# Kernel optimization log

Measured on AMD Instinct MI355X. Metric: run time of the kernel, lower is better.

Reference implementation:

```python
import jax, jax.numpy as jnp
import numpy as np

N = 100000
E = 3200000
EMBED = 64
RBF = 16
EPS_ANGLE = 1e-8
EPS_NORM = 1e-12  # F.normalize default eps


def _linear(h, W, b):
    return h @ W + b


def setup_inputs() -> dict:
    key = jax.random.key(0)
    ks = jax.random.split(key, 12)
    s = lambda fan_in: 1.0 / np.sqrt(fan_in)
    return {
        "x": jax.random.normal(ks[0], (N, EMBED), jnp.float32),
        "coord": jax.random.normal(ks[1], (N, 3), jnp.float32),
        "rbf_feature": jax.random.normal(ks[2], (E, RBF), jnp.float32),
        "edge_index": jax.random.randint(ks[3], (2, E), 0, N, jnp.int64),
        # edge_mlp: Linear(RBF+1, EMBED) -> SiLU -> Linear(EMBED, EMBED)
        "W1": jax.random.uniform(ks[4], (RBF + 1, EMBED), jnp.float32, -s(RBF + 1), s(RBF + 1)),
        "b1": jnp.zeros((EMBED,), jnp.float32),
        "W2": jax.random.uniform(ks[5], (EMBED, EMBED), jnp.float32, -s(EMBED), s(EMBED)),
        "b2": jnp.zeros((EMBED,), jnp.float32),
        # update_mlp: Linear(EMBED, EMBED) -> SiLU -> Linear(EMBED, EMBED)
        "W3": jax.random.uniform(ks[6], (EMBED, EMBED), jnp.float32, -s(EMBED), s(EMBED)),
        "b3": jnp.zeros((EMBED,), jnp.float32),
        "W4": jax.random.uniform(ks[7], (EMBED, EMBED), jnp.float32, -s(EMBED), s(EMBED)),
        "b4": jnp.zeros((EMBED,), jnp.float32),
    }


def reference(x, coord, rbf_feature, edge_index, W1, b1, W2, b2, W3, b3, W4, b4):
    row, col = edge_index[0], edge_index[1]
    # gather per-edge displacement vectors: [E, 3]
    v = coord[row] - coord[col]
    # compute_angle(v, -v): normalize both, cosine, clamp, acos
    norm = jnp.maximum(jnp.linalg.norm(v, axis=-1, keepdims=True), EPS_NORM)
    vn = v / norm
    cos_angle = jnp.clip(jnp.sum(vn * (-vn), axis=-1), -1.0 + EPS_ANGLE, 1.0 - EPS_ANGLE)
    angle = jnp.arccos(cos_angle)[:, None]  # [E, 1]
    edge_feat = jnp.concatenate([rbf_feature, angle], axis=-1)  # [E, RBF+1]
    # edge MLP
    edge_msg = _linear(jax.nn.silu(_linear(edge_feat, W1, b1)), W2, b2)  # [E, EMBED]
    # scatter-add to source nodes (index_add_ over row)
    agg = jax.ops.segment_sum(edge_msg, row, num_segments=x.shape[0])  # [N, EMBED]
    # node update
    return x + _linear(jax.nn.silu(_linear(agg, W3, b3)), W4, b4)
```

## Files before the change

kernel.cpp:

```cpp
#include <hip/hip_runtime.h>
#include <hip/hip_fp16.h>
#include <hip/hip_bf16.h>

typedef __attribute__((ext_vector_type(8)))  short bf16x8;
typedef __attribute__((ext_vector_type(4)))  float f32x4;
typedef __attribute__((ext_vector_type(16))) float f32x16;

constexpr int EMBED = 64;
constexpr int RBF   = 16;

__device__ __forceinline__ short f2bf(float f) {
    __hip_bfloat16 h = __float2bfloat16(f);
    return *reinterpret_cast<short*>(&h);
}
__device__ __forceinline__ float bf2f(short s) {
    unsigned u = ((unsigned)(unsigned short)s) << 16;
    return __uint_as_float(u);
}
__device__ __forceinline__ unsigned pk_bf(float lo, float hi) {
    unsigned l = (unsigned short)f2bf(lo);
    unsigned h = (unsigned short)f2bf(hi);
    return l | (h << 16);
}
__device__ __forceinline__ unsigned pk_f16(float lo, float hi) {
    __half2 h = __halves2half2(__float2half_rn(lo), __float2half_rn(hi));
    return *reinterpret_cast<unsigned*>(&h);
}
__device__ __forceinline__ void atom_pk_add_f16(__half* addr, unsigned data) {
    asm volatile("global_atomic_pk_add_f16 %0, %1, off"
                 :: "v"(addr), "v"(data) : "memory");
}
__device__ __forceinline__ float silu(float x) {
    return x * __builtin_amdgcn_rcpf(1.0f + __expf(-x));
}

constexpr float PI_BF  = 3.140625f;
constexpr float PI2_BF = 1.5703125f;

__device__ __forceinline__ int crow(int j, int h) {
    return (j & 3) + 8 * (j >> 2) + 4 * h;
}

template <bool GUARD, bool F16>
__global__ __launch_bounds__(256, 2) void edge_kernel32(
    const float* __restrict__ rbf,
    const int* __restrict__ ei,
    const float* __restrict__ W1,
    const float* __restrict__ b1,
    const float* __restrict__ W2,
    const float* __restrict__ b2,
    void* __restrict__ agg,
    int e_base, int E)
{
    __shared__ __align__(16) short lds_s[4][32 * 64];
    __shared__ int lds_row[256];
    __shared__ unsigned char lds_flag[256];
    __shared__ int wave_any[4];

    const int tid  = threadIdx.x;
    const int lane = tid & 63;
    const int wave = tid >> 6;
    const int n = lane & 31;
    const int h = lane >> 5;
    const int blk_e0 = e_base + blockIdx.x * 256;

    {
        const int e = blk_e0 + tid;
        const bool v = !GUARD || (e < E);
        const int row = v ? ei[e] : 0;
        const int col = v ? ei[E + e] : 1;
        lds_row[tid]  = row;
        const bool fl = v && (row == col);
        lds_flag[tid] = fl;
        const unsigned long long m = __ballot(fl);
        if (lane == 0) wave_any[wave] = (m != 0ull);
    }
    __syncthreads();

    bf16x8 b1f[2];
    float  b1v[2], dlt[2], b2v[2];
#pragma unroll
    for (int hh = 0; hh < 2; ++hh) {
        const int ch = 2 * n + hh;
#pragma unroll
        for (int j = 0; j < 8; ++j)
            b1f[hh][j] = f2bf(W1[(h * 8 + j) * EMBED + ch]);
        const float w16 = bf2f(f2bf(W1[RBF * EMBED + ch]));
        b1v[hh] = b1[ch] + PI_BF * w16;
        dlt[hh] = (PI2_BF - PI_BF) * w16;
        b2v[hh] = b2[ch];
    }
    bf16x8 b2f[4][2];
#pragma unroll
    for (int kk = 0; kk < 4; ++kk)
#pragma unroll
        for (int hh = 0; hh < 2; ++hh) {
            const int ch = 2 * n + hh;
#pragma unroll
            for (int j = 0; j < 8; ++j)
                b2f[kk][hh][j] = f2bf(W2[(kk * 16 + h * 8 + j) * EMBED + ch]);
        }

    char* const sl = reinterpret_cast<char*>(lds_s[wave]);

#pragma unroll 1
    for (int mt = 0; mt < 2; ++mt) {
        const int e0  = blk_e0 + wave * 64 + mt * 32;
        if (GUARD && e0 >= E) break;
        const int el0 = wave * 64 + mt * 32;

        bf16x8 a1 = {};
        {
            const int ea = e0 + n;
            if (!GUARD || ea < E) {
                const float4 p0 = *reinterpret_cast<const float4*>(rbf + (long long)ea * RBF + h * 8);
                const float4 p1 = *reinterpret_cast<const float4*>(rbf + (long long)ea * RBF + h * 8 + 4);
                a1[0] = f2bf(p0.x); a1[1] = f2bf(p0.y); a1[2] = f2bf(p0.z); a1[3] = f2bf(p0.w);
                a1[4] = f2bf(p1.x); a1[5] = f2bf(p1.y); a1[6] = f2bf(p1.z); a1[7] = f2bf(p1.w);
            }
        }

        f32x16 accA, accB;
#pragma unroll
        for (int j = 0; j < 16; ++j) { accA[j] = b1v[0]; accB[j] = b1v[1]; }
        accA = __builtin_amdgcn_mfma_f32_32x32x16_bf16(a1, b1f[0], accA, 0, 0, 0);
        accB = __builtin_amdgcn_mfma_f32_32x32x16_bf16(a1, b1f[1], accB, 0, 0, 0);

        if (wave_any[wave]) {
#pragma unroll
            for (int j = 0; j < 16; ++j) {
                const int m = crow(j, h);
                if (lds_flag[el0 + m]) { accA[j] += dlt[0]; accB[j] += dlt[1]; }
            }
        }

#pragma unroll
        for (int j = 0; j < 16; ++j) {
            const int m = crow(j, h);
            const unsigned u = pk_bf(silu(accA[j]), silu(accB[j]));
            *reinterpret_cast<unsigned*>(sl + m * 128 + ((4 * n) ^ ((m & 7) << 4))) = u;
        }
        __builtin_amdgcn_wave_barrier();

        f32x16 acc2A, acc2B;
#pragma unroll
        for (int j = 0; j < 16; ++j) { acc2A[j] = b2v[0]; acc2B[j] = b2v[1]; }
#pragma unroll
        for (int kk = 0; kk < 4; ++kk) {
            const int byte = n * 128 + ((kk * 32 + h * 16) ^ ((n & 7) << 4));
            const bf16x8 a2 = *reinterpret_cast<const bf16x8*>(sl + byte);
            acc2A = __builtin_amdgcn_mfma_f32_32x32x16_bf16(a2, b2f[kk][0], acc2A, 0, 0, 0);
            acc2B = __builtin_amdgcn_mfma_f32_32x32x16_bf16(a2, b2f[kk][1], acc2B, 0, 0, 0);
        }
        __builtin_amdgcn_wave_barrier();

#pragma unroll
        for (int j = 0; j < 16; ++j) {
            const int m = crow(j, h);
            const int eat = e0 + m;
            if (!GUARD || eat < E) {
                const unsigned row = (unsigned)lds_row[el0 + m];
                if (F16) {
                    __half* const dst = reinterpret_cast<__half*>(agg) + row * 64u;
                    atom_pk_add_f16(dst + 2 * n, pk_f16(acc2A[j], acc2B[j]));
                } else {
                    float* const dst = reinterpret_cast<float*>(agg) + row * 64u;
                    atomicAdd(dst + 2 * n,     acc2A[j]);
                    atomicAdd(dst + 2 * n + 1, acc2B[j]);
                }
            }
        }
    }
}

template <bool F16>
__global__ __launch_bounds__(256) void node_kernel(
    const float* __restrict__ x, const void* __restrict__ aggv,
    const float* __restrict__ W3, const float* __restrict__ b3,
    const float* __restrict__ W4, const float* __restrict__ b4,
    float* __restrict__ out, int nn)
{
    __shared__ __align__(16) float lds_s[4][EMBED];
    const int lane = threadIdx.x & 63;
    const int wave = threadIdx.x >> 6;
    float w3c[EMBED], w4c[EMBED];
#pragma unroll
    for (int j = 0; j < EMBED; ++j) w3c[j] = W3[j * EMBED + lane];
#pragma unroll
    for (int j = 0; j < EMBED; ++j) w4c[j] = W4[j * EMBED + lane];
    const float b3v = b3[lane];
    const float b4v = b4[lane];
    const float4* s4 = reinterpret_cast<const float4*>(lds_s[wave]);
    const int wid = blockIdx.x * 4 + wave;
    const int nw  = gridDim.x * 4;
    for (int n = wid; n < nn; n += nw) {
        const long long base = (long long)n * EMBED + lane;
        float a;
        if (F16) a = __half2float(reinterpret_cast<const __half*>(aggv)[base]);
        else     a = reinterpret_cast<const float*>(aggv)[base];
        lds_s[wave][lane] = a;
        __builtin_amdgcn_wave_barrier();
        float acc = b3v;
#pragma unroll
        for (int j4 = 0; j4 < EMBED / 4; ++j4) {
            const float4 sv = s4[j4];
            acc = fmaf(sv.x, w3c[4 * j4 + 0], acc);
            acc = fmaf(sv.y, w3c[4 * j4 + 1], acc);
            acc = fmaf(sv.z, w3c[4 * j4 + 2], acc);
            acc = fmaf(sv.w, w3c[4 * j4 + 3], acc);
        }
        const float s = acc * __builtin_amdgcn_rcpf(1.0f + __expf(-acc));
        __builtin_amdgcn_wave_barrier();
        lds_s[wave][lane] = s;
        __builtin_amdgcn_wave_barrier();
        float acc2 = b4v;
#pragma unroll
        for (int j4 = 0; j4 < EMBED / 4; ++j4) {
            const float4 sv = s4[j4];
            acc2 = fmaf(sv.x, w4c[4 * j4 + 0], acc2);
            acc2 = fmaf(sv.y, w4c[4 * j4 + 1], acc2);
            acc2 = fmaf(sv.z, w4c[4 * j4 + 2], acc2);
            acc2 = fmaf(sv.w, w4c[4 * j4 + 3], acc2);
        }
        __builtin_amdgcn_wave_barrier();
        out[base] = x[base] + acc2;
    }
}

extern "C" void kernel_launch(void* const* d_in, const int* in_sizes, int n_in,
                              void* d_out, int out_size, void* d_ws, size_t ws_size,
                              hipStream_t stream) {
    const float* x      = (const float*)d_in[0];
    const float* rbf    = (const float*)d_in[2];
    const int*   ei     = (const int*)d_in[3];
    const float* W1 = (const float*)d_in[4];
    const float* b1 = (const float*)d_in[5];
    const float* W2 = (const float*)d_in[6];
    const float* b2 = (const float*)d_in[7];
    const float* W3 = (const float*)d_in[8];
    const float* b3 = (const float*)d_in[9];
    const float* W4 = (const float*)d_in[10];
    const float* b4 = (const float*)d_in[11];
    float* out = (float*)d_out;

    const int E  = (int)(in_sizes[3] / 2);
    const int nn = in_sizes[0] / EMBED;

    void* agg16 = d_ws;
    const size_t neededF16 = (size_t)nn * EMBED * sizeof(__half);

    const int nfull = E / 256;
    const int rem   = E - nfull * 256;

    if (ws_size >= neededF16) {
        hipMemsetAsync(agg16, 0, neededF16, stream);
        if (nfull)
            edge_kernel32<false, true><<<dim3(nfull), dim3(256), 0, stream>>>(
                rbf, ei, W1, b1, W2, b2, agg16, 0, E);
        if (rem)
            edge_kernel32<true, true><<<dim3(1), dim3(256), 0, stream>>>(
                rbf, ei, W1, b1, W2, b2, agg16, nfull * 256, E);
        node_kernel<true><<<dim3(2048), dim3(256), 0, stream>>>(
            x, agg16, W3, b3, W4, b4, out, nn);
    } else {
        hipMemsetAsync(out, 0, (size_t)nn * EMBED * sizeof(float), stream);
        if (nfull)
            edge_kernel32<false, false><<<dim3(nfull), dim3(256), 0, stream>>>(
                rbf, ei, W1, b1, W2, b2, out, 0, E);
        if (rem)
            edge_kernel32<true, false><<<dim3(1), dim3(256), 0, stream>>>(
                rbf, ei, W1, b1, W2, b2, out, nfull * 256, E);
        node_kernel<false><<<dim3(2048), dim3(256), 0, stream>>>(
            x, out, W3, b3, W4, b4, out, nn);
    }
}
```

Measured before the change: 394.8 us.

## Replace atomic scatter-add with counting-sort by row and segmented reduction

Adds a histogram and three-pass prefix scan over source-node indices, then has the edge kernel write each fp16 message into a row-sorted slot buffer instead of atomically adding into a node accumulator. A new node kernel reduces each node's contiguous segment and applies the update MLP in one pass. This removes the per-element fp16 atomics but adds about 400MB of message writes and reads plus extra launches and per-edge cursor atomics. It also needs a large workspace, falling back to the old path when the workspace is too small.

```diff
diff --git a/kernel.cpp b/kernel.cpp
--- a/kernel.cpp
+++ b/kernel.cpp
@@ -8,6 +8,7 @@
 
 constexpr int EMBED = 64;
 constexpr int RBF   = 16;
+constexpr int SCAN_TILE = 1024;
 
 __device__ __forceinline__ short f2bf(float f) {
     __hip_bfloat16 h = __float2bfloat16(f);
@@ -41,19 +42,82 @@
     return (j & 3) + 8 * (j >> 2) + 4 * h;
 }
 
-template <bool GUARD, bool F16>
-__global__ __launch_bounds__(256, 2) void edge_kernel32(
+__global__ __launch_bounds__(256) void k_hist(
+    const int* __restrict__ ei, int* __restrict__ counts, int E)
+{
+    int i = blockIdx.x * 256 + threadIdx.x;
+    if (i < E) atomicAdd(&counts[ei[i]], 1);
+}
+
+__global__ __launch_bounds__(256) void k_scan1(
+    const int* __restrict__ counts, int* __restrict__ offsets,
+    int* __restrict__ bsums, int nn)
+{
+    __shared__ int lds[256];
+    const int t = threadIdx.x;
+    const int base = blockIdx.x * SCAN_TILE;
+    int v[4]; int s = 0;
+#pragma unroll
+    for (int j = 0; j < 4; ++j) {
+        const int i = base + t * 4 + j;
+        v[j] = (i < nn) ? counts[i] : 0;
+        s += v[j];
+    }
+    lds[t] = s;
+    __syncthreads();
+    for (int off = 1; off < 256; off <<= 1) {
+        int x = (t >= off) ? lds[t - off] : 0;
+        __syncthreads();
+        lds[t] += x;
+        __syncthreads();
+    }
+    int run = lds[t] - s;
+    if (t == 255) bsums[blockIdx.x] = lds[255];
+#pragma unroll
+    for (int j = 0; j < 4; ++j) {
+        const int i = base + t * 4 + j;
+        if (i < nn) offsets[i] = run;
+        run += v[j];
+    }
+}
+
+__global__ void k_scan2(int* __restrict__ bsums, int nblk)
+{
+    if (threadIdx.x == 0 && blockIdx.x == 0) {
+        int a = 0;
+        for (int i = 0; i < nblk; ++i) { int t = bsums[i]; bsums[i] = a; a += t; }
+    }
+}
+
+__global__ __launch_bounds__(256) void k_scan3(
+    int* __restrict__ offsets, const int* __restrict__ bsums,
+    int* __restrict__ counts, int nn, int Etot)
+{
+    const int base = blockIdx.x * SCAN_TILE;
+    const int add = bsums[blockIdx.x];
+#pragma unroll
+    for (int j = 0; j < 4; ++j) {
+        const int i = base + threadIdx.x * 4 + j;
+        if (i < nn) { offsets[i] += add; counts[i] = 0; }
+    }
+    if (blockIdx.x == 0 && threadIdx.x == 0) offsets[nn] = Etot;
+}
+
+template <bool GUARD>
+__global__ __launch_bounds__(256, 2) void edge_kernel_sort(
     const float* __restrict__ rbf,
     const int* __restrict__ ei,
     const float* __restrict__ W1,
     const float* __restrict__ b1,
     const float* __restrict__ W2,
     const float* __restrict__ b2,
-    void* __restrict__ agg,
+    const int* __restrict__ offsets,
+    int* __restrict__ cursor,
+    unsigned* __restrict__ smsg,
     int e_base, int E)
 {
     __shared__ __align__(16) short lds_s[4][32 * 64];
-    __shared__ int lds_row[256];
+    __shared__ int lds_slot[256];
     __shared__ unsigned char lds_flag[256];
     __shared__ int wave_any[4];
 
@@ -69,7 +133,9 @@
         const bool v = !GUARD || (e < E);
         const int row = v ? ei[e] : 0;
         const int col = v ? ei[E + e] : 1;
-        lds_row[tid]  = row;
+        int slot = 0;
+        if (v) slot = offsets[row] + atomicAdd(&cursor[row], 1);
+        lds_slot[tid] = slot;
         const bool fl = v && (row == col);
         lds_flag[tid] = fl;
         const unsigned long long m = __ballot(fl);
@@ -154,6 +220,187 @@
         }
         __builtin_amdgcn_wave_barrier();
 
+#pragma unroll
+        for (int j = 0; j < 16; ++j) {
+            const int m = crow(j, h);
+            const int eat = e0 + m;
+            if (!GUARD || eat < E) {
+                const size_t slot = (size_t)lds_slot[el0 + m];
+                smsg[slot * 32u + (unsigned)n] = pk_f16(acc2A[j], acc2B[j]);
+            }
+        }
+    }
+}
+
+__global__ __launch_bounds__(256) void seg_node_kernel(
+    const float* __restrict__ x,
+    const unsigned* __restrict__ smsg,
+    const int* __restrict__ offsets,
+    const float* __restrict__ W3, const float* __restrict__ b3,
+    const float* __restrict__ W4, const float* __restrict__ b4,
+    float* __restrict__ out, int nn)
+{
+    __shared__ __align__(16) float lds_s[4][EMBED];
+    const int lane = threadIdx.x & 63;
+    const int wave = threadIdx.x >> 6;
+    const int dw = lane & 31;
+    const int rp = lane >> 5;
+
+    float w3c[EMBED], w4c[EMBED];
+#pragma unroll
+    for (int j = 0; j < EMBED; ++j) w3c[j] = W3[j * EMBED + lane];
+#pragma unroll
+    for (int j = 0; j < EMBED; ++j) w4c[j] = W4[j * EMBED + lane];
+    const float b3v = b3[lane];
+    const float b4v = b4[lane];
+
+    const float4* s4 = reinterpret_cast<const float4*>(lds_s[wave]);
+    const int wid = blockIdx.x * 4 + wave;
+    const int nw  = gridDim.x * 4;
+
+    for (int n = wid; n < nn; n += nw) {
+        const int beg = offsets[n];
+        const int end = offsets[n + 1];
+
+        float s0 = 0.0f, s1 = 0.0f;
+#pragma unroll 4
+        for (int j = beg + rp; j < end; j += 2) {
+            const unsigned d = smsg[(size_t)j * 32u + (unsigned)dw];
+            const __half2 h2 = *reinterpret_cast<const __half2*>(&d);
+            s0 += __low2float(h2);
+            s1 += __high2float(h2);
+        }
+        s0 += __shfl_xor(s0, 32, 64);
+        s1 += __shfl_xor(s1, 32, 64);
+
+        lds_s[wave][2 * dw]     = s0;
+        lds_s[wave][2 * dw + 1] = s1;
+        __builtin_amdgcn_wave_barrier();
+
+        float acc = b3v;
+#pragma unroll
+        for (int j4 = 0; j4 < EMBED / 4; ++j4) {
+            const float4 sv = s4[j4];
+            acc = fmaf(sv.x, w3c[4 * j4 + 0], acc);
+            acc = fmaf(sv.y, w3c[4 * j4 + 1], acc);
+            acc = fmaf(sv.z, w3c[4 * j4 + 2], acc);
+            acc = fmaf(sv.w, w3c[4 * j4 + 3], acc);
+        }
+        const float s = acc * __builtin_amdgcn_rcpf(1.0f + __expf(-acc));
+        __builtin_amdgcn_wave_barrier();
+        lds_s[wave][lane] = s;
+        __builtin_amdgcn_wave_barrier();
+        float acc2 = b4v;
+#pragma unroll
+        for (int j4 = 0; j4 < EMBED / 4; ++j4) {
+            const float4 sv = s4[j4];
+            acc2 = fmaf(sv.x, w4c[4 * j4 + 0], acc2);
+            acc2 = fmaf(sv.y, w4c[4 * j4 + 1], acc2);
+            acc2 = fmaf(sv.z, w4c[4 * j4 + 2], acc2);
+            acc2 = fmaf(sv.w, w4c[4 * j4 + 3], acc2);
+        }
+        __builtin_amdgcn_wave_barrier();
+
+        const long long base = (long long)n * EMBED + lane;
+        out[base] = x[base] + acc2;
+    }
+}
+
+template <bool GUARD, bool F16>
+__global__ __launch_bounds__(256, 2) void edge_kernel32(
+    const float* __restrict__ rbf, const int* __restrict__ ei,
+    const float* __restrict__ W1, const float* __restrict__ b1,
+    const float* __restrict__ W2, const float* __restrict__ b2,
+    void* __restrict__ agg, int e_base, int E)
+{
+    __shared__ __align__(16) short lds_s[4][32 * 64];
+    __shared__ int lds_row[256];
+    __shared__ unsigned char lds_flag[256];
+    __shared__ int wave_any[4];
+    const int tid = threadIdx.x, lane = tid & 63, wave = tid >> 6;
+    const int n = lane & 31, h = lane >> 5;
+    const int blk_e0 = e_base + blockIdx.x * 256;
+    {
+        const int e = blk_e0 + tid;
+        const bool v = !GUARD || (e < E);
+        const int row = v ? ei[e] : 0;
+        const int col = v ? ei[E + e] : 1;
+        lds_row[tid] = row;
+        const bool fl = v && (row == col);
+        lds_flag[tid] = fl;
+        const unsigned long long m = __ballot(fl);
+        if (lane == 0) wave_any[wave] = (m != 0ull);
+    }
+    __syncthreads();
+    bf16x8 b1f[2];
+    float b1v[2], dlt[2], b2v[2];
+#pragma unroll
+    for (int hh = 0; hh < 2; ++hh) {
+        const int ch = 2 * n + hh;
+#pragma unroll
+        for (int j = 0; j < 8; ++j)
+            b1f[hh][j] = f2bf(W1[(h * 8 + j) * EMBED + ch]);
+        const float w16 = bf2f(f2bf(W1[RBF * EMBED + ch]));
+        b1v[hh] = b1[ch] + PI_BF * w16;
+        dlt[hh] = (PI2_BF - PI_BF) * w16;
+        b2v[hh] = b2[ch];
+    }
+    bf16x8 b2f[4][2];
+#pragma unroll
+    for (int kk = 0; kk < 4; ++kk)
+#pragma unroll
+        for (int hh = 0; hh < 2; ++hh) {
+            const int ch = 2 * n + hh;
+#pragma unroll
+            for (int j = 0; j < 8; ++j)
+                b2f[kk][hh][j] = f2bf(W2[(kk * 16 + h * 8 + j) * EMBED + ch]);
+        }
+    char* const sl = reinterpret_cast<char*>(lds_s[wave]);
+#pragma unroll 1
+    for (int mt = 0; mt < 2; ++mt) {
+        const int e0 = blk_e0 + wave * 64 + mt * 32;
+        if (GUARD && e0 >= E) break;
+        const int el0 = wave * 64 + mt * 32;
+        bf16x8 a1 = {};
+        {
+            const int ea = e0 + n;
+            if (!GUARD || ea < E) {
+                const float4 p0 = *reinterpret_cast<const float4*>(rbf + (long long)ea * RBF + h * 8);
+                const float4 p1 = *reinterpret_cast<const float4*>(rbf + (long long)ea * RBF + h * 8 + 4);
+                a1[0] = f2bf(p0.x); a1[1] = f2bf(p0.y); a1[2] = f2bf(p0.z); a1[3] = f2bf(p0.w);
+                a1[4] = f2bf(p1.x); a1[5] = f2bf(p1.y); a1[6] = f2bf(p1.z); a1[7] = f2bf(p1.w);
+            }
+        }
+        f32x16 accA, accB;
+#pragma unroll
+        for (int j = 0; j < 16; ++j) { accA[j] = b1v[0]; accB[j] = b1v[1]; }
+        accA = __builtin_amdgcn_mfma_f32_32x32x16_bf16(a1, b1f[0], accA, 0, 0, 0);
+        accB = __builtin_amdgcn_mfma_f32_32x32x16_bf16(a1, b1f[1], accB, 0, 0, 0);
+        if (wave_any[wave]) {
+#pragma unroll
+            for (int j = 0; j < 16; ++j) {
+                const int m = crow(j, h);
+                if (lds_flag[el0 + m]) { accA[j] += dlt[0]; accB[j] += dlt[1]; }
+            }
+        }
+#pragma unroll
+        for (int j = 0; j < 16; ++j) {
+            const int m = crow(j, h);
+            const unsigned u = pk_bf(silu(accA[j]), silu(accB[j]));
+            *reinterpret_cast<unsigned*>(sl + m * 128 + ((4 * n) ^ ((m & 7) << 4))) = u;
+        }
+        __builtin_amdgcn_wave_barrier();
+        f32x16 acc2A, acc2B;
+#pragma unroll
+        for (int j = 0; j < 16; ++j) { acc2A[j] = b2v[0]; acc2B[j] = b2v[1]; }
+#pragma unroll
+        for (int kk = 0; kk < 4; ++kk) {
+            const int byte = n * 128 + ((kk * 32 + h * 16) ^ ((n & 7) << 4));
+            const bf16x8 a2 = *reinterpret_cast<const bf16x8*>(sl + byte);
+            acc2A = __builtin_amdgcn_mfma_f32_32x32x16_bf16(a2, b2f[kk][0], acc2A, 0, 0, 0);
+            acc2B = __builtin_amdgcn_mfma_f32_32x32x16_bf16(a2, b2f[kk][1], acc2B, 0, 0, 0);
+        }
+        __builtin_amdgcn_wave_barrier();
 #pragma unroll
         for (int j = 0; j < 16; ++j) {
             const int m = crow(j, h);
@@ -245,23 +492,44 @@
 
     const int E  = (int)(in_sizes[3] / 2);
     const int nn = in_sizes[0] / EMBED;
-
-    void* agg16 = d_ws;
-    const size_t neededF16 = (size_t)nn * EMBED * sizeof(__half);
+    const int nscan = (nn + SCAN_TILE - 1) / SCAN_TILE;
+    const int nsPad = (nscan + 63) & ~63;
+
+    const size_t msgBytes = (size_t)E * 128;
+    unsigned* smsg  = (unsigned*)d_ws;
+    int* offsets    = (int*)((char*)d_ws + msgBytes);
+    int* counts     = offsets + nn + 1;
+    int* bsums      = counts + nn;
+    const size_t neededSort = msgBytes + sizeof(int) * ((size_t)(nn + 1) + nn + nsPad);
 
     const int nfull = E / 256;
     const int rem   = E - nfull * 256;
-
-    if (ws_size >= neededF16) {
-        hipMemsetAsync(agg16, 0, neededF16, stream);
+    const unsigned egrid = (unsigned)((E + 255) / 256);
+
+    if (ws_size >= neededSort) {
+        hipMemsetAsync(counts, 0, sizeof(int) * nn, stream);
+        k_hist<<<dim3(egrid), dim3(256), 0, stream>>>(ei, counts, E);
+        k_scan1<<<dim3((unsigned)nscan), dim3(256), 0, stream>>>(counts, offsets, bsums, nn);
+        k_scan2<<<dim3(1), dim3(64), 0, stream>>>(bsums, nscan);
+        k_scan3<<<dim3((unsigned)nscan), dim3(256), 0, stream>>>(offsets, bsums, counts, nn, E);
+        if (nfull)
+            edge_kernel_sort<false><<<dim3(nfull), dim3(256), 0, stream>>>(
+                rbf, ei, W1, b1, W2, b2, offsets, counts, smsg, 0, E);
+        if (rem)
+            edge_kernel_sort<true><<<dim3(1), dim3(256), 0, stream>>>(
+                rbf, ei, W1, b1, W2, b2, offsets, counts, smsg, nfull * 256, E);
+        seg_node_kernel<<<dim3(2048), dim3(256), 0, stream>>>(
+            x, smsg, offsets, W3, b3, W4, b4, out, nn);
+    } else if (ws_size >= (size_t)nn * EMBED * sizeof(__half)) {
+        hipMemsetAsync(d_ws, 0, (size_t)nn * EMBED * sizeof(__half), stream);
         if (nfull)
             edge_kernel32<false, true><<<dim3(nfull), dim3(256), 0, stream>>>(
-                rbf, ei, W1, b1, W2, b2, agg16, 0, E);
+                rbf, ei, W1, b1, W2, b2, d_ws, 0, E);
         if (rem)
             edge_kernel32<true, true><<<dim3(1), dim3(256), 0, stream>>>(
-                rbf, ei, W1, b1, W2, b2, agg16, nfull * 256, E);
+                rbf, ei, W1, b1, W2, b2, d_ws, nfull * 256, E);
         node_kernel<true><<<dim3(2048), dim3(256), 0, stream>>>(
-            x, agg16, W3, b3, W4, b4, out, nn);
+            x, d_ws, W3, b3, W4, b4, out, nn);
     } else {
         hipMemsetAsync(out, 0, (size_t)nn * EMBED * sizeof(float), stream);
         if (nfull)
```

New measurement: 641.7 us. 1.63x slower.
